# Optimization experiments

Measured on AMD Instinct MI355X. Metric: run time of the kernel, lower is better.

## Reference

```python
import jax, jax.numpy as jnp
import numpy as np

N, M, K, C = 1000, 2000, 10, 80
IOU_THRESHOLD = 0.5
EPS = 1e-7


def setup_inputs() -> dict:
    key = jax.random.key(0)
    k1, k2, k3, k4, k5, k6, k7 = jax.random.split(key, 7)
    # pred boxes: realistic xyxy boxes in a 1000x1000 image
    cxy = jax.random.uniform(k1, (N, 2), minval=0.0, maxval=1000.0)
    wh = jax.random.uniform(k2, (N, 2), minval=20.0, maxval=100.0)
    pred_box = jnp.concatenate([cxy - wh / 2, cxy + wh / 2], axis=1)  # [N,4]
    pred = jnp.concatenate([pred_box, jax.random.uniform(k3, (N, 2))], axis=1)  # [N,6]
    # dropout passes: jittered copies of pred boxes (guarantees IoU>0.5 match)
    # followed by M-N random boxes
    copies = pred_box[None, :, :] + jax.random.normal(k4, (K, N, 4)) * 1.0  # [K,N,4]
    rc = jax.random.uniform(k5, (K, M - N, 2), minval=0.0, maxval=1000.0)
    rwh = jax.random.uniform(k6, (K, M - N, 2), minval=20.0, maxval=100.0)
    rand_box = jnp.concatenate([rc - rwh / 2, rc + rwh / 2], axis=2)  # [K,M-N,4]
    boxes = jnp.concatenate([copies, rand_box], axis=1)  # [K,M,4]
    dropout_preds = jnp.concatenate([boxes, jnp.ones((K, M, 2), jnp.float32)], axis=2)
    # per-box class probability rows (softmax-normalized, strictly positive)
    dropout_cls_confs = jax.nn.softmax(jax.random.normal(k7, (K, M, C)), axis=-1)
    return {
        "pred": pred.astype(jnp.float32),
        "dropout_preds": dropout_preds.astype(jnp.float32),
        "dropout_cls_confs": dropout_cls_confs.astype(jnp.float32),
    }


def _pairwise_iou(b1, b2):
    # b1: [N,4] xyxy, b2: [K,M,4] xyxy -> iou [K,N,M]
    ix1 = jnp.maximum(b1[None, :, None, 0], b2[:, None, :, 0])
    iy1 = jnp.maximum(b1[None, :, None, 1], b2[:, None, :, 1])
    ix2 = jnp.minimum(b1[None, :, None, 2], b2[:, None, :, 2])
    iy2 = jnp.minimum(b1[None, :, None, 3], b2[:, None, :, 3])
    inter = jnp.clip(ix2 - ix1, 0.0) * jnp.clip(iy2 - iy1, 0.0)  # [K,N,M]
    area1 = (b1[:, 2] - b1[:, 0]) * (b1[:, 3] - b1[:, 1])  # [N]
    area2 = (b2[..., 2] - b2[..., 0]) * (b2[..., 3] - b2[..., 1])  # [K,M]
    return inter / (area1[None, :, None] + area2[:, None, :] - inter + EPS)


def reference(pred, dropout_preds, dropout_cls_confs):
    n_classes = dropout_cls_confs.shape[-1]
    inv_n = 1.0 / n_classes
    max_entropy = -n_classes * (inv_n * jnp.log(jnp.float32(inv_n)))  # == log(C)

    iou = _pairwise_iou(pred[:, :4], dropout_preds[:, :, :4])  # [K,N,M]
    mask = iou > IOU_THRESHOLD  # [K,N,M]
    matched = jnp.any(mask, axis=-1)  # [K,N] any match in pass k for pred n
    first = jnp.argmax(mask, axis=-1)  # [K,N] index of FIRST match (break semantics)

    # gather the matched class-confidence row per (pass, pred): [K,N,C]
    rows = jnp.take_along_axis(dropout_cls_confs, first[:, :, None], axis=1)
    entropy = -jnp.sum(rows * jnp.log(rows), axis=-1)  # [K,N]
    u = 1.0 - entropy / max_entropy  # [K,N]

    matched_f = matched.astype(u.dtype)
    cnt = jnp.sum(matched_f, axis=0)  # [N]
    sum_u = jnp.sum(u * matched_f, axis=0)  # [N]
    # no-match fallback in original yields NaN (entropy of zeros row)
    semantic_uncertainty = jnp.where(cnt > 0, sum_u / jnp.maximum(cnt, 1.0), jnp.nan)
    return semantic_uncertainty
```

## Files before the change

### kernel.cpp

```cpp
#include <hip/hip_runtime.h>
#include <math.h>

#define N_PRED 1000
#define M_BOX  2000
#define K_PASS 10
#define C_CLS  80
#define IOU_THR 0.5f
#define EPS_IOU 1e-7f

__global__ __launch_bounds__(K_PASS * 64)
void ue_cls_kernel(const float* __restrict__ pred,
                   const float* __restrict__ dpreds,
                   const float* __restrict__ dconfs,
                   float* __restrict__ out)
{
    const int n    = blockIdx.x;
    const int wave = threadIdx.x >> 6;
    const int lane = threadIdx.x & 63;
    const int k    = wave;

    __shared__ float s_u[K_PASS];
    __shared__ float s_m[K_PASS];

    const float px1 = pred[n * 6 + 0];
    const float py1 = pred[n * 6 + 1];
    const float px2 = pred[n * 6 + 2];
    const float py2 = pred[n * 6 + 3];
    const float area1 = (px2 - px1) * (py2 - py1);

    const long baseRow = (long)k * M_BOX;
    const float2* dp2 = (const float2*)dpreds;
    int first = -1;
    for (int c0 = 0; c0 < M_BOX; c0 += 64) {
        const int m = c0 + lane;
        bool hit = false;
        if (m < M_BOX) {
            const long i2 = (baseRow + m) * 3;
            const float2 a = dp2[i2];
            const float2 b = dp2[i2 + 1];
            const float bx1 = a.x, by1 = a.y, bx2 = b.x, by2 = b.y;
            const float ix1 = fmaxf(px1, bx1);
            const float iy1 = fmaxf(py1, by1);
            const float ix2 = fminf(px2, bx2);
            const float iy2 = fminf(py2, by2);
            const float inter = fmaxf(ix2 - ix1, 0.0f) * fmaxf(iy2 - iy1, 0.0f);
            const float area2 = (bx2 - bx1) * (by2 - by1);
            const float iou = inter / (area1 + area2 - inter + EPS_IOU);
            hit = iou > IOU_THR;
        }
        const unsigned long long bal = __ballot(hit);
        if (bal) { first = c0 + __builtin_ctzll(bal); break; }
    }

    float u = 0.0f, matched = 0.0f;
    if (first >= 0) {
        matched = 1.0f;
        const float* row = dconfs + (baseRow + first) * C_CLS;
        float local = 0.0f;
        {
            const float p = row[lane];
            local -= p * logf(p);
        }
        if (lane < C_CLS - 64) {
            const float q = row[64 + lane];
            local -= q * logf(q);
        }
        #pragma unroll
        for (int off = 32; off > 0; off >>= 1)
            local += __shfl_xor(local, off, 64);
        const float inv_n  = 1.0f / (float)C_CLS;
        const float max_en = -(float)C_CLS * (inv_n * logf(inv_n));
        u = 1.0f - local / max_en;
    }

    if (lane == 0) { s_u[k] = u * matched; s_m[k] = matched; }
    __syncthreads();

    if (threadIdx.x == 0) {
        float cnt = 0.0f, su = 0.0f;
        #pragma unroll
        for (int kk = 0; kk < K_PASS; ++kk) { cnt += s_m[kk]; su += s_u[kk]; }
        out[n] = (cnt > 0.0f) ? (su / fmaxf(cnt, 1.0f)) : __builtin_nanf("");
    }
}

extern "C" void kernel_launch(void* const* d_in, const int* in_sizes, int n_in,
                              void* d_out, int out_size, void* d_ws, size_t ws_size,
                              hipStream_t stream) {
    const float* pred   = (const float*)d_in[0];
    const float* dpreds = (const float*)d_in[1];
    const float* dconfs = (const float*)d_in[2];
    float* out = (float*)d_out;

    ue_cls_kernel<<<dim3(N_PRED), dim3(K_PASS * 64), 0, stream>>>(pred, dpreds, dconfs, out);
}
```

Before: 73.37 us.

## Stage pass boxes in LDS per block and split reduction into second kernel

The grid is reorganized so each block handles one dropout pass and a group of ten predictions. All 2000 boxes of that pass are staged once into shared memory, and every wave scans them from LDS. The early-exit ballot loop becomes a full unrolled scan with a min-reduction over lanes, which trades the early break for more instruction-level parallelism. Per-pass results go to a workspace, and a small second kernel averages over passes, which adds a launch and 32KB of LDS per block.

```diff
diff --git a/kernel.cpp b/kernel.cpp
--- a/kernel.cpp
+++ b/kernel.cpp
@@ -8,19 +8,33 @@
 #define IOU_THR 0.5f
 #define EPS_IOU 1e-7f
 
-__global__ __launch_bounds__(K_PASS * 64)
-void ue_cls_kernel(const float* __restrict__ pred,
-                   const float* __restrict__ dpreds,
-                   const float* __restrict__ dconfs,
-                   float* __restrict__ out)
+#define G_PRED 10
+#define BLK_T  (G_PRED * 64)
+#define NBLK_PER_K (N_PRED / G_PRED)
+
+__global__ __launch_bounds__(BLK_T)
+void ue_pass_kernel(const float* __restrict__ pred,
+                    const float* __restrict__ dpreds,
+                    const float* __restrict__ dconfs,
+                    float2* __restrict__ ws)
 {
-    const int n    = blockIdx.x;
+    __shared__ float4 s_box[M_BOX];
+
+    const int bk   = blockIdx.x;
+    const int k    = bk / NBLK_PER_K;
+    const int g    = bk % NBLK_PER_K;
     const int wave = threadIdx.x >> 6;
     const int lane = threadIdx.x & 63;
-    const int k    = wave;
+    const int n    = g * G_PRED + wave;
 
-    __shared__ float s_u[K_PASS];
-    __shared__ float s_m[K_PASS];
+    const float2* dp2 = (const float2*)dpreds;
+    const long kbase = (long)k * M_BOX;
+    for (int i = threadIdx.x; i < M_BOX; i += BLK_T) {
+        const float2 a = dp2[(kbase + i) * 3];
+        const float2 b = dp2[(kbase + i) * 3 + 1];
+        s_box[i] = make_float4(a.x, a.y, b.x, b.y);
+    }
+    __syncthreads();
 
     const float px1 = pred[n * 6 + 0];
     const float py1 = pred[n * 6 + 1];
@@ -28,34 +42,28 @@
     const float py2 = pred[n * 6 + 3];
     const float area1 = (px2 - px1) * (py2 - py1);
 
-    const long baseRow = (long)k * M_BOX;
-    const float2* dp2 = (const float2*)dpreds;
-    int first = -1;
+    int firstIdx = 0x7fffffff;
+    #pragma unroll 4
     for (int c0 = 0; c0 < M_BOX; c0 += 64) {
         const int m = c0 + lane;
-        bool hit = false;
-        if (m < M_BOX) {
-            const long i2 = (baseRow + m) * 3;
-            const float2 a = dp2[i2];
-            const float2 b = dp2[i2 + 1];
-            const float bx1 = a.x, by1 = a.y, bx2 = b.x, by2 = b.y;
-            const float ix1 = fmaxf(px1, bx1);
-            const float iy1 = fmaxf(py1, by1);
-            const float ix2 = fminf(px2, bx2);
-            const float iy2 = fminf(py2, by2);
-            const float inter = fmaxf(ix2 - ix1, 0.0f) * fmaxf(iy2 - iy1, 0.0f);
-            const float area2 = (bx2 - bx1) * (by2 - by1);
-            const float iou = inter / (area1 + area2 - inter + EPS_IOU);
-            hit = iou > IOU_THR;
-        }
-        const unsigned long long bal = __ballot(hit);
-        if (bal) { first = c0 + __builtin_ctzll(bal); break; }
+        const float4 bx = s_box[m < M_BOX ? m : (M_BOX - 1)];
+        const float ix1 = fmaxf(px1, bx.x);
+        const float iy1 = fmaxf(py1, bx.y);
+        const float ix2 = fminf(px2, bx.z);
+        const float iy2 = fminf(py2, bx.w);
+        const float inter = fmaxf(ix2 - ix1, 0.0f) * fmaxf(iy2 - iy1, 0.0f);
+        const float area2 = (bx.z - bx.x) * (bx.w - bx.y);
+        const float iou = inter / (area1 + area2 - inter + EPS_IOU);
+        if (iou > IOU_THR && m < M_BOX) firstIdx = min(firstIdx, m);
     }
+    #pragma unroll
+    for (int off = 32; off > 0; off >>= 1)
+        firstIdx = min(firstIdx, __shfl_xor(firstIdx, off, 64));
 
-    float u = 0.0f, matched = 0.0f;
-    if (first >= 0) {
-        matched = 1.0f;
-        const float* row = dconfs + (baseRow + first) * C_CLS;
+    float um = 0.0f, mt = 0.0f;
+    if (firstIdx != 0x7fffffff) {
+        mt = 1.0f;
+        const float* row = dconfs + (kbase + firstIdx) * (long)C_CLS;
         float local = 0.0f;
         {
             const float p = row[lane];
@@ -70,18 +78,25 @@
             local += __shfl_xor(local, off, 64);
         const float inv_n  = 1.0f / (float)C_CLS;
         const float max_en = -(float)C_CLS * (inv_n * logf(inv_n));
-        u = 1.0f - local / max_en;
+        um = 1.0f - local / max_en;
     }
 
-    if (lane == 0) { s_u[k] = u * matched; s_m[k] = matched; }
-    __syncthreads();
+    if (lane == 0) ws[(long)k * N_PRED + n] = make_float2(um, mt);
+}
 
-    if (threadIdx.x == 0) {
-        float cnt = 0.0f, su = 0.0f;
-        #pragma unroll
-        for (int kk = 0; kk < K_PASS; ++kk) { cnt += s_m[kk]; su += s_u[kk]; }
-        out[n] = (cnt > 0.0f) ? (su / fmaxf(cnt, 1.0f)) : __builtin_nanf("");
+__global__ __launch_bounds__(256)
+void ue_reduce_kernel(const float2* __restrict__ ws, float* __restrict__ out)
+{
+    const int n = blockIdx.x * blockDim.x + threadIdx.x;
+    if (n >= N_PRED) return;
+    float cnt = 0.0f, su = 0.0f;
+    #pragma unroll
+    for (int k = 0; k < K_PASS; ++k) {
+        const float2 v = ws[(long)k * N_PRED + n];
+        su  += v.x;
+        cnt += v.y;
     }
+    out[n] = (cnt > 0.0f) ? (su / fmaxf(cnt, 1.0f)) : __builtin_nanf("");
 }
 
 extern "C" void kernel_launch(void* const* d_in, const int* in_sizes, int n_in,
@@ -90,7 +105,10 @@
     const float* pred   = (const float*)d_in[0];
     const float* dpreds = (const float*)d_in[1];
     const float* dconfs = (const float*)d_in[2];
-    float* out = (float*)d_out;
+    float* out  = (float*)d_out;
+    float2* ws  = (float2*)d_ws;
 
-    ue_cls_kernel<<<dim3(N_PRED), dim3(K_PASS * 64), 0, stream>>>(pred, dpreds, dconfs, out);
+    ue_pass_kernel<<<dim3(K_PASS * NBLK_PER_K), dim3(BLK_T), 0, stream>>>(
+        pred, dpreds, dconfs, ws);
+    ue_reduce_kernel<<<dim3((N_PRED + 255) / 256), dim3(256), 0, stream>>>(ws, out);
 }
```

After: 84.15 us. +14.7%, slower.

## Process two predictions per block with full branchless IoU scan

Applied to the files above, without the earlier changes.

Each block now handles two prediction boxes, so every loaded dropout box is tested against both predictions and the box loads are shared. The early-exit ballot scan is replaced by a full unrolled scan over all M boxes that keeps a per-lane minimum matching index, followed by a cross-lane min-reduction. This removes the per-chunk ballot and branch but gives up the early break, so every wave now scans all 2000 boxes even when the first match comes early. The grid also shrinks to half as many blocks.

```diff
diff --git a/kernel.cpp b/kernel.cpp
--- a/kernel.cpp
+++ b/kernel.cpp
@@ -8,79 +8,103 @@
 #define IOU_THR 0.5f
 #define EPS_IOU 1e-7f
 
-__global__ __launch_bounds__(K_PASS * 64)
+#define P_PRED 2
+#define BLK_T  (K_PASS * 64)
+#define N_BLK  (N_PRED / P_PRED)
+
+__global__ __launch_bounds__(BLK_T)
 void ue_cls_kernel(const float* __restrict__ pred,
                    const float* __restrict__ dpreds,
                    const float* __restrict__ dconfs,
                    float* __restrict__ out)
 {
-    const int n    = blockIdx.x;
-    const int wave = threadIdx.x >> 6;
+    const int k    = threadIdx.x >> 6;
     const int lane = threadIdx.x & 63;
-    const int k    = wave;
+    const int n0   = blockIdx.x * P_PRED;
 
-    __shared__ float s_u[K_PASS];
-    __shared__ float s_m[K_PASS];
+    __shared__ float s_u[K_PASS][P_PRED];
+    __shared__ float s_m[K_PASS][P_PRED];
 
-    const float px1 = pred[n * 6 + 0];
-    const float py1 = pred[n * 6 + 1];
-    const float px2 = pred[n * 6 + 2];
-    const float py2 = pred[n * 6 + 3];
-    const float area1 = (px2 - px1) * (py2 - py1);
+    float px1[P_PRED], py1[P_PRED], px2[P_PRED], py2[P_PRED], a1[P_PRED];
+    #pragma unroll
+    for (int p = 0; p < P_PRED; ++p) {
+        const float* pr = pred + (n0 + p) * 6;
+        px1[p] = pr[0]; py1[p] = pr[1]; px2[p] = pr[2]; py2[p] = pr[3];
+        a1[p] = (px2[p] - px1[p]) * (py2[p] - py1[p]);
+    }
 
-    const long baseRow = (long)k * M_BOX;
+    const long kbase = (long)k * M_BOX;
     const float2* dp2 = (const float2*)dpreds;
-    int first = -1;
+    int firstI[P_PRED];
+    #pragma unroll
+    for (int p = 0; p < P_PRED; ++p) firstI[p] = 0x7fffffff;
+
+    #pragma unroll 4
     for (int c0 = 0; c0 < M_BOX; c0 += 64) {
         const int m = c0 + lane;
-        bool hit = false;
-        if (m < M_BOX) {
-            const long i2 = (baseRow + m) * 3;
-            const float2 a = dp2[i2];
-            const float2 b = dp2[i2 + 1];
-            const float bx1 = a.x, by1 = a.y, bx2 = b.x, by2 = b.y;
-            const float ix1 = fmaxf(px1, bx1);
-            const float iy1 = fmaxf(py1, by1);
-            const float ix2 = fminf(px2, bx2);
-            const float iy2 = fminf(py2, by2);
+        const bool valid = (m < M_BOX);
+        const long i2 = (kbase + (valid ? m : M_BOX - 1)) * 3;
+        const float2 a = dp2[i2];
+        const float2 b = dp2[i2 + 1];
+        const float area2 = (b.x - a.x) * (b.y - a.y);
+        #pragma unroll
+        for (int p = 0; p < P_PRED; ++p) {
+            const float ix1 = fmaxf(px1[p], a.x);
+            const float iy1 = fmaxf(py1[p], a.y);
+            const float ix2 = fminf(px2[p], b.x);
+            const float iy2 = fminf(py2[p], b.y);
             const float inter = fmaxf(ix2 - ix1, 0.0f) * fmaxf(iy2 - iy1, 0.0f);
-            const float area2 = (bx2 - bx1) * (by2 - by1);
-            const float iou = inter / (area1 + area2 - inter + EPS_IOU);
-            hit = iou > IOU_THR;
+            const float iou = inter / (a1[p] + area2 - inter + EPS_IOU);
+            if (valid && iou > IOU_THR) firstI[p] = min(firstI[p], m);
         }
-        const unsigned long long bal = __ballot(hit);
-        if (bal) { first = c0 + __builtin_ctzll(bal); break; }
+    }
+    #pragma unroll
+    for (int off = 32; off > 0; off >>= 1) {
+        #pragma unroll
+        for (int p = 0; p < P_PRED; ++p)
+            firstI[p] = min(firstI[p], __shfl_xor(firstI[p], off, 64));
     }
 
-    float u = 0.0f, matched = 0.0f;
-    if (first >= 0) {
-        matched = 1.0f;
-        const float* row = dconfs + (baseRow + first) * C_CLS;
-        float local = 0.0f;
-        {
-            const float p = row[lane];
-            local -= p * logf(p);
+    const float inv_n  = 1.0f / (float)C_CLS;
+    const float max_en = -(float)C_CLS * (inv_n * logf(inv_n));
+    float um[P_PRED], mt[P_PRED];
+    #pragma unroll
+    for (int p = 0; p < P_PRED; ++p) {
+        um[p] = 0.0f; mt[p] = 0.0f;
+        if (firstI[p] != 0x7fffffff) {
+            mt[p] = 1.0f;
+            const float* row = dconfs + (kbase + firstI[p]) * (long)C_CLS;
+            float local = 0.0f;
+            {
+                const float v = row[lane];
+                local -= v * logf(v);
+            }
+            if (lane < C_CLS - 64) {
+                const float v = row[64 + lane];
+                local -= v * logf(v);
+            }
+            #pragma unroll
+            for (int off = 32; off > 0; off >>= 1)
+                local += __shfl_xor(local, off, 64);
+            um[p] = 1.0f - local / max_en;
         }
-        if (lane < C_CLS - 64) {
-            const float q = row[64 + lane];
-            local -= q * logf(q);
-        }
-        #pragma unroll
-        for (int off = 32; off > 0; off >>= 1)
-            local += __shfl_xor(local, off, 64);
-        const float inv_n  = 1.0f / (float)C_CLS;
-        const float max_en = -(float)C_CLS * (inv_n * logf(inv_n));
-        u = 1.0f - local / max_en;
     }
 
-    if (lane == 0) { s_u[k] = u * matched; s_m[k] = matched; }
+    if (lane == 0) {
+        #pragma unroll
+        for (int p = 0; p < P_PRED; ++p) {
+            s_u[k][p] = um[p] * mt[p];
+            s_m[k][p] = mt[p];
+        }
+    }
     __syncthreads();
 
-    if (threadIdx.x == 0) {
+    if (threadIdx.x < P_PRED) {
+        const int t = threadIdx.x;
         float cnt = 0.0f, su = 0.0f;
         #pragma unroll
-        for (int kk = 0; kk < K_PASS; ++kk) { cnt += s_m[kk]; su += s_u[kk]; }
-        out[n] = (cnt > 0.0f) ? (su / fmaxf(cnt, 1.0f)) : __builtin_nanf("");
+        for (int kk = 0; kk < K_PASS; ++kk) { su += s_u[kk][t]; cnt += s_m[kk][t]; }
+        out[n0 + t] = (cnt > 0.0f) ? (su / fmaxf(cnt, 1.0f)) : __builtin_nanf("");
     }
 }
 
@@ -92,5 +116,5 @@
     const float* dconfs = (const float*)d_in[2];
     float* out = (float*)d_out;
 
-    ue_cls_kernel<<<dim3(N_PRED), dim3(K_PASS * 64), 0, stream>>>(pred, dpreds, dconfs, out);
+    ue_cls_kernel<<<dim3(N_BLK), dim3(BLK_T), 0, stream>>>(pred, dpreds, dconfs, out);
 }
```

Measured after the change: 82.11 us. 11.9% more time.
